# Kernel optimization log

Measured on AMD Instinct MI355X. Metric: run time of the kernel, lower is better.

Reference implementation:

```python
import jax, jax.numpy as jnp
import numpy as np

N = 50000       # total nodes
D = 20000       # disease nodes (first D rows)
M = 30000       # mirna nodes
E = 800000      # edges
DSIM = 512; MSIM = 512
HID = 128; OUT = 128; P = 3   # powers p = [0,1,2]
PAIRS = 100000


def _lin(k, o, i):
    s = 1.0 / np.sqrt(i)
    return jax.random.uniform(k, (o, i), jnp.float32, -s, s)


def setup_inputs() -> dict:
    key = jax.random.key(0)
    ks = jax.random.split(key, 24)
    inp = {}
    inp["d_sim"] = jax.random.normal(ks[0], (N, DSIM), jnp.float32)
    inp["m_sim"] = jax.random.normal(ks[1], (N, MSIM), jnp.float32)
    inp["edge_src"] = jax.random.randint(ks[2], (E,), 0, N, jnp.int32)
    inp["edge_dst"] = jax.random.randint(ks[3], (E,), 0, N, jnp.int32)
    inp["src"] = jax.random.randint(ks[4], (PAIRS,), 0, D, jnp.int32)
    inp["dst"] = D + jax.random.randint(ks[5], (PAIRS,), 0, M, jnp.int32)
    # input projections
    inp["d_fc_w"] = _lin(ks[6], HID, DSIM); inp["d_fc_b"] = jnp.zeros((HID,), jnp.float32)
    inp["m_fc_w"] = _lin(ks[7], HID, MSIM); inp["m_fc_b"] = jnp.zeros((HID,), jnp.float32)
    # MixHopConv per-power weights (no bias)
    inp["l0_w"] = jnp.stack([_lin(ks[8 + j], OUT, HID) for j in range(P)])         # [P, OUT, HID]
    inp["l1_w"] = jnp.stack([_lin(ks[11 + j], HID, OUT * P) for j in range(P)])    # [P, HID, OUT*P]
    inp["fc_w"] = _lin(ks[14], OUT, HID * P)
    inp["d_fc1_w"] = _lin(ks[15], OUT, OUT + DSIM); inp["d_fc1_b"] = jnp.zeros((OUT,), jnp.float32)
    inp["m_fc1_w"] = _lin(ks[16], OUT, OUT + MSIM); inp["m_fc1_b"] = jnp.zeros((OUT,), jnp.float32)
    # predictor MLP
    inp["p0_w"] = _lin(ks[17], OUT, 2 * OUT); inp["p0_b"] = jnp.zeros((OUT,), jnp.float32)
    inp["p1_w"] = _lin(ks[18], 1, OUT); inp["p1_b"] = jnp.zeros((1,), jnp.float32)
    return inp


def _mixhop(feats, Ws, edge_src, edge_dst, norm):
    """DGL MixHopConv with p=[0,1,2]: outputs [W_j (D^-1/2 A D^-1/2)^j X for j in p], concatenated."""
    outs = []
    for j in range(P):
        outs.append(feats @ Ws[j].T)
        if j < P - 1:  # propagate one more hop (last hop's propagation is unused)
            feats = feats * norm
            feats = jax.ops.segment_sum(feats[edge_src], edge_dst, num_segments=N)
            feats = feats * norm
    return jnp.concatenate(outs, axis=1)


def reference(d_sim, m_sim, edge_src, edge_dst, src, dst,
              d_fc_w, d_fc_b, m_fc_w, m_fc_b, l0_w, l1_w, fc_w,
              d_fc1_w, d_fc1_b, m_fc1_w, m_fc1_b, p0_w, p0_b, p1_w, p1_b):
    # symmetric normalization from in-degrees (clamped to >= 1)
    degs = jax.ops.segment_sum(jnp.ones((E,), jnp.float32), edge_dst, num_segments=N)
    norm = (jnp.maximum(degs, 1.0) ** -0.5)[:, None]  # [N, 1]
    # per-node-type input projection (dropout = identity in eval)
    z_d = d_sim[:D] @ d_fc_w.T + d_fc_b
    z_m = m_sim[D:] @ m_fc_w.T + m_fc_b
    feats = jnp.concatenate([z_d, z_m], axis=0)               # [N, HID]
    feats = _mixhop(feats, l0_w, edge_src, edge_dst, norm)    # [N, OUT*P]
    feats = _mixhop(feats, l1_w, edge_src, edge_dst, norm)    # [N, HID*P]
    feats = feats @ fc_w.T                                    # [N, OUT]
    h_d = jax.nn.elu(jnp.concatenate([feats[:D], d_sim[:D]], axis=1) @ d_fc1_w.T + d_fc1_b)
    h_m = jax.nn.elu(jnp.concatenate([feats[D:], m_sim[D:]], axis=1) @ m_fc1_w.T + m_fc1_b)
    h = jnp.concatenate([h_d, h_m], axis=0)                   # [N, OUT]
    hc = jnp.concatenate([h[src], h[dst]], axis=1)            # [PAIRS, 2*OUT]
    score = jax.nn.sigmoid(jax.nn.relu(hc @ p0_w.T + p0_b) @ p1_w.T + p1_b)
    return score
```

## Files before the change

kernel.cpp:

```cpp
#include <hip/hip_runtime.h>
#include <cstddef>
#include <cstdint>

#define N_NODES 50000
#define D_NODES 20000
#define M_NODES 30000
#define E_EDGES 800000
#define PAIRS_N 100000

typedef unsigned short u16;
typedef unsigned int u32;
typedef short bf16x8 __attribute__((ext_vector_type(8)));
typedef float f32x4 __attribute__((ext_vector_type(4)));

__device__ __forceinline__ float bf2f(u16 u) {
  u32 v = ((u32)u) << 16;
  return __builtin_bit_cast(float, v);
}
__device__ __forceinline__ u16 f2bf(float f) {
  u32 u = __builtin_bit_cast(u32, f);
  u32 r = (u + 0x7fffu + ((u >> 16) & 1u)) >> 16;
  return (u16)r;
}
__device__ __forceinline__ u32 pk2(float x, float y) {
  return (u32)f2bf(x) | ((u32)f2bf(y) << 16);
}

__global__ void wconv_kernel(const float* s0, const float* s1, const float* s2,
                             const float* s3, const float* s4,
                             u16* d0, u16* d1, u16* d2, u16* d3, u16* d4) {
  int i = blockIdx.x * 256 + threadIdx.x;
  const float* s; u16* d; int l;
  if      (i < 16384) { s = s0; d = d0; l = i; }
  else if (i < 32768) { s = s1; d = d1; l = i - 16384; }
  else if (i < 53248) { s = s2; d = d2; l = i - 32768; }
  else if (i < 73728) { s = s3; d = d3; l = i - 53248; }
  else if (i < 81920) { s = s4; d = d4; l = i - 73728; }
  else return;
  float4 v = *(const float4*)(s + (size_t)l * 4);
  ushort4 o;
  o.x = f2bf(v.x); o.y = f2bf(v.y); o.z = f2bf(v.z); o.w = f2bf(v.w);
  *(ushort4*)(d + (size_t)l * 4) = o;
}

__global__ void wcomb1_kernel(const float* __restrict__ l1w, const float* __restrict__ l0w,
                              float* __restrict__ Tmp) {
  int pj = blockIdx.x;
  int p = pj / 3, j = pj % 3;
  int o = blockIdx.y;
  int i = threadIdx.x;
  const float* wp = l1w + (size_t)p * 49152 + (size_t)o * 384 + 128 * j;
  const float* wj = l0w + (size_t)j * 16384 + i;
  float acc = 0.f;
#pragma unroll 4
  for (int t = 0; t < 128; ++t) acc += wp[t] * wj[(size_t)t * 128];
  Tmp[(size_t)pj * 16384 + (size_t)o * 128 + i] = acc;
}
__global__ void wcomb2_kernel(const float* __restrict__ fcw, const float* __restrict__ Tmp,
                              u16* __restrict__ G) {
  int k = blockIdx.x;
  int of = blockIdx.y;
  int i = threadIdx.x;
  float acc = 0.f;
  int plo = (k > 2) ? (k - 2) : 0;
  int phi = (k < 2) ? k : 2;
  for (int p = plo; p <= phi; ++p) {
    int j = k - p;
    const float* fp = fcw + (size_t)of * 384 + 128 * p;
    const float* tp = Tmp + (size_t)(p * 3 + j) * 16384 + i;
#pragma unroll 4
    for (int t = 0; t < 128; ++t) acc += fp[t] * tp[(size_t)t * 128];
  }
  G[(size_t)of * 640 + 128 * k + i] = f2bf(acc);
}

__global__ void deg_count_kernel(const int* __restrict__ dst, int* __restrict__ degs, int e) {
  int i = blockIdx.x * 256 + threadIdx.x;
  if (i < e) atomicAdd(&degs[dst[i]], 1);
}
__global__ void norm_reduce_kernel(const int* __restrict__ degs, float* __restrict__ norm,
                                   int n, int* __restrict__ bsums) {
  __shared__ int s[256];
  int t = threadIdx.x;
  int i = blockIdx.x * 256 + t;
  int d = (i < n) ? degs[i] : 0;
  if (i < n) norm[i] = rsqrtf(fmaxf((float)d, 1.0f));
  s[t] = d;
  __syncthreads();
  for (int st = 128; st > 0; st >>= 1) {
    if (t < st) s[t] += s[t + st];
    __syncthreads();
  }
  if (t == 0) bsums[blockIdx.x] = s[0];
}
__global__ void scan_small_kernel(int* b, int nb) {
  __shared__ int s[256];
  int t = threadIdx.x;
  int orig = (t < nb) ? b[t] : 0;
  s[t] = orig;
  __syncthreads();
  for (int st = 1; st < 256; st <<= 1) {
    int v = (t >= st) ? s[t - st] : 0;
    __syncthreads();
    s[t] += v;
    __syncthreads();
  }
  if (t < nb) b[t] = s[t] - orig;
}
__global__ void scan_final_kernel(const int* __restrict__ degs, const int* __restrict__ boff,
                                  int* __restrict__ out, int* __restrict__ cursor,
                                  int n, int total) {
  __shared__ int s[256];
  int t = threadIdx.x;
  int i = blockIdx.x * 256 + t;
  int orig = (i < n) ? degs[i] : 0;
  s[t] = orig;
  __syncthreads();
  for (int st = 1; st < 256; st <<= 1) {
    int v = (t >= st) ? s[t - st] : 0;
    __syncthreads();
    s[t] += v;
    __syncthreads();
  }
  if (i < n) {
    int v = boff[blockIdx.x] + s[t] - orig;
    out[i] = v;
    cursor[i] = v;
  }
  if (i == 0) out[n] = total;
}
__global__ void fill_csr_kernel(const int* __restrict__ esrc, const int* __restrict__ edst,
                                int* __restrict__ cursor, int* __restrict__ csr_src, int e) {
  int i = blockIdx.x * 256 + threadIdx.x;
  if (i < e) {
    int p = atomicAdd(&cursor[edst[i]], 1);
    csr_src[p] = esrc[i];
  }
}

__global__ void prop_kernel(const u16* __restrict__ in,
                            u16* __restrict__ outu, int ldu, int cOff,
                            u16* __restrict__ outs,
                            const int* __restrict__ off, const int* __restrict__ srcs,
                            const float* __restrict__ norm, int nnodes) {
  const int node = blockIdx.x * 4 + (threadIdx.x >> 6);
  if (node >= nnodes) return;
  const int lane = threadIdx.x & 63;
  const int e0 = off[node], e1 = off[node + 1];
  float a0 = 0.f, a1 = 0.f;
  const u16* basec = in + (lane << 1);
  for (int base = e0; base < e1; base += 64) {
    int nE = e1 - base; if (nE > 64) nE = 64;
    int myE = srcs[base + ((lane < nE) ? lane : (nE - 1))];
    int i = 0;
    for (; i + 8 <= nE; i += 8) {
      int s0 = __builtin_amdgcn_readlane(myE, i + 0);
      int s1 = __builtin_amdgcn_readlane(myE, i + 1);
      int s2 = __builtin_amdgcn_readlane(myE, i + 2);
      int s3 = __builtin_amdgcn_readlane(myE, i + 3);
      int s4 = __builtin_amdgcn_readlane(myE, i + 4);
      int s5 = __builtin_amdgcn_readlane(myE, i + 5);
      int s6 = __builtin_amdgcn_readlane(myE, i + 6);
      int s7 = __builtin_amdgcn_readlane(myE, i + 7);
      u32 v0 = *(const u32*)(basec + ((size_t)s0 << 7));
      u32 v1 = *(const u32*)(basec + ((size_t)s1 << 7));
      u32 v2 = *(const u32*)(basec + ((size_t)s2 << 7));
      u32 v3 = *(const u32*)(basec + ((size_t)s3 << 7));
      u32 v4 = *(const u32*)(basec + ((size_t)s4 << 7));
      u32 v5 = *(const u32*)(basec + ((size_t)s5 << 7));
      u32 v6 = *(const u32*)(basec + ((size_t)s6 << 7));
      u32 v7 = *(const u32*)(basec + ((size_t)s7 << 7));
      a0 += bf2f((u16)v0); a1 += bf2f((u16)(v0 >> 16));
      a0 += bf2f((u16)v1); a1 += bf2f((u16)(v1 >> 16));
      a0 += bf2f((u16)v2); a1 += bf2f((u16)(v2 >> 16));
      a0 += bf2f((u16)v3); a1 += bf2f((u16)(v3 >> 16));
      a0 += bf2f((u16)v4); a1 += bf2f((u16)(v4 >> 16));
      a0 += bf2f((u16)v5); a1 += bf2f((u16)(v5 >> 16));
      a0 += bf2f((u16)v6); a1 += bf2f((u16)(v6 >> 16));
      a0 += bf2f((u16)v7); a1 += bf2f((u16)(v7 >> 16));
    }
    for (; i < nE; ++i) {
      int s = __builtin_amdgcn_readlane(myE, i);
      u32 v = *(const u32*)(basec + ((size_t)s << 7));
      a0 += bf2f((u16)v); a1 += bf2f((u16)(v >> 16));
    }
  }
  float nd = norm[node];
  *(u32*)(outu + (size_t)node * ldu + cOff + (lane << 1)) = pk2(a0 * nd, a1 * nd);
  if (outs) {
    float nd2 = nd * nd;
    *(u32*)(outs + ((size_t)node << 7) + (lane << 1)) = pk2(a0 * nd2, a1 * nd2);
  }
}

__global__ __launch_bounds__(256) void mfma_gemm_kernel(
    const void* __restrict__ A1a, const void* __restrict__ A1b, int lda1, int K1, int a1f32,
    const void* __restrict__ A2a, const void* __restrict__ A2b, int lda2, int K2, int a2f32,
    const int* __restrict__ gsrc, const int* __restrict__ gdst,
    const u16* __restrict__ Wa, const u16* __restrict__ Wb,
    const float* __restrict__ biasa, const float* __restrict__ biasb,
    int splitB, int rowD, int boundA, int nrows,
    u16* __restrict__ Cu, int ldcu, int colOff,
    u16* __restrict__ Cs, const float* __restrict__ normp,
    const float* __restrict__ p1w, const float* __restrict__ p1b, float* __restrict__ outf,
    int act) {
  __shared__ u32 As[32 * 32];
  __shared__ u32 Ws[128 * 32];
  const int tid = threadIdx.x;
  const bool segb = (int)blockIdx.x >= splitB;
  const int brow = segb ? rowD + ((int)blockIdx.x - splitB) * 32 : (int)blockIdx.x * 32;
  const int bound = segb ? nrows : boundA;
  const void* A1 = segb ? A1b : A1a;
  const void* A2 = segb ? A2b : A2a;
  const u16* W = segb ? Wb : Wa;
  const float* bias = segb ? biasb : biasa;
  const int K = K1 + K2;
  const int lane = tid & 63;
  const int wv = tid >> 6;
  const int fr = lane & 15;
  const int fg = lane >> 4;

  f32x4 acc[2][2];
#pragma unroll
  for (int m = 0; m < 2; ++m)
#pragma unroll
    for (int n = 0; n < 2; ++n) acc[m][n] = (f32x4){0.f, 0.f, 0.f, 0.f};

  const int sr = tid >> 3, sk = tid & 7;
  const int swc = tid >> 1, sh = tid & 1;
  const int prow = (brow + sr < bound) ? (brow + sr) : (bound - 1);

  for (int kc = 0; kc < K; kc += 64) {
    uint4 qa;
    {
      bool seg1 = kc < K1;
      int kk = (seg1 ? kc : kc - K1) + sk * 8;
      const void* Av = seg1 ? A1 : A2;
      int ld = seg1 ? lda1 : lda2;
      int isf = seg1 ? a1f32 : a2f32;
      int row = gsrc ? (seg1 ? gsrc[prow] : gdst[prow]) : prow;
      if (isf) {
        const float* p = (const float*)Av + (size_t)row * ld + kk;
        float4 f0 = ((const float4*)p)[0];
        float4 f1 = ((const float4*)p)[1];
        qa = make_uint4(pk2(f0.x, f0.y), pk2(f0.z, f0.w), pk2(f1.x, f1.y), pk2(f1.z, f1.w));
      } else {
        qa = *(const uint4*)((const u16*)Av + (size_t)row * ld + kk);
      }
    }
    const u16* wp = W + (size_t)swc * K + kc + sh * 32;
    uint4 qw0 = *(const uint4*)(wp);
    uint4 qw1 = *(const uint4*)(wp + 8);
    uint4 qw2 = *(const uint4*)(wp + 16);
    uint4 qw3 = *(const uint4*)(wp + 24);

    __syncthreads();
    *(uint4*)&As[sr * 32 + (sk ^ (sr & 7)) * 4] = qa;
    *(uint4*)&Ws[swc * 32 + ((sh * 4 + 0) ^ (swc & 7)) * 4] = qw0;
    *(uint4*)&Ws[swc * 32 + ((sh * 4 + 1) ^ (swc & 7)) * 4] = qw1;
    *(uint4*)&Ws[swc * 32 + ((sh * 4 + 2) ^ (swc & 7)) * 4] = qw2;
    *(uint4*)&Ws[swc * 32 + ((sh * 4 + 3) ^ (swc & 7)) * 4] = qw3;
    __syncthreads();

#pragma unroll
    for (int kk2 = 0; kk2 < 2; ++kk2) {
      int gix = kk2 * 4 + fg;
      int r0 = fr, r1 = 16 + fr;
      bf16x8 aF0 = *(const bf16x8*)&As[r0 * 32 + (gix ^ (r0 & 7)) * 4];
      bf16x8 aF1 = *(const bf16x8*)&As[r1 * 32 + (gix ^ (r1 & 7)) * 4];
#pragma unroll
      for (int n = 0; n < 2; ++n) {
        int cr = wv * 32 + n * 16 + fr;
        bf16x8 bF = *(const bf16x8*)&Ws[cr * 32 + (gix ^ (cr & 7)) * 4];
        acc[0][n] = __builtin_amdgcn_mfma_f32_16x16x32_bf16(aF0, bF, acc[0][n], 0, 0, 0);
        acc[1][n] = __builtin_amdgcn_mfma_f32_16x16x32_bf16(aF1, bF, acc[1][n], 0, 0, 0);
      }
    }
  }

  if (act == 3) {
    float part[2][4];
#pragma unroll
    for (int m = 0; m < 2; ++m)
#pragma unroll
      for (int i = 0; i < 4; ++i) part[m][i] = 0.f;
#pragma unroll
    for (int n = 0; n < 2; ++n) {
      int ccol = wv * 32 + n * 16 + fr;
      float b = bias[ccol];
      float pw = p1w[ccol];
#pragma unroll
      for (int m = 0; m < 2; ++m)
#pragma unroll
        for (int i = 0; i < 4; ++i) {
          float v = acc[m][n][i] + b;
          v = fmaxf(v, 0.f);
          part[m][i] += v * pw;
        }
    }
#pragma unroll
    for (int mask = 1; mask <= 8; mask <<= 1)
#pragma unroll
      for (int m = 0; m < 2; ++m)
#pragma unroll
        for (int i = 0; i < 4; ++i) part[m][i] += __shfl_xor(part[m][i], mask);
    __syncthreads();
    float* sred = (float*)As;
    if (fr == 0) {
#pragma unroll
      for (int m = 0; m < 2; ++m)
#pragma unroll
        for (int i = 0; i < 4; ++i) sred[wv * 32 + m * 16 + fg * 4 + i] = part[m][i];
    }
    __syncthreads();
    if (tid < 32) {
      int row = brow + tid;
      if (row < bound) {
        float s = sred[tid] + sred[32 + tid] + sred[64 + tid] + sred[96 + tid] + p1b[0];
        outf[row] = 1.f / (1.f + expf(-s));
      }
    }
    return;
  }

#pragma unroll
  for (int m = 0; m < 2; ++m) {
#pragma unroll
    for (int n = 0; n < 2; ++n) {
      int ccol = wv * 32 + n * 16 + fr;
      float b = bias ? bias[ccol] : 0.f;
#pragma unroll
      for (int i = 0; i < 4; ++i) {
        int row = brow + m * 16 + fg * 4 + i;
        if (row < bound) {
          float v = acc[m][n][i] + b;
          if (act == 1) v = (v > 0.f) ? v : (expf(v) - 1.f);
          else if (act == 2) v = fmaxf(v, 0.f);
          Cu[(size_t)row * ldcu + colOff + ccol] = f2bf(v);
          if (Cs) Cs[((size_t)row << 7) + ccol] = f2bf(v * normp[row]);
        }
      }
    }
  }
}

extern "C" void kernel_launch(void* const* d_in, const int* in_sizes, int n_in,
                              void* d_out, int out_size, void* d_ws, size_t ws_size,
                              hipStream_t stream) {
  const float* d_sim   = (const float*)d_in[0];
  const float* m_sim   = (const float*)d_in[1];
  const int*   e_src   = (const int*)d_in[2];
  const int*   e_dst   = (const int*)d_in[3];
  const int*   p_src   = (const int*)d_in[4];
  const int*   p_dst   = (const int*)d_in[5];
  const float* d_fc_w  = (const float*)d_in[6];
  const float* d_fc_b  = (const float*)d_in[7];
  const float* m_fc_w  = (const float*)d_in[8];
  const float* m_fc_b  = (const float*)d_in[9];
  const float* l0_w    = (const float*)d_in[10];
  const float* l1_w    = (const float*)d_in[11];
  const float* fc_w    = (const float*)d_in[12];
  const float* d_fc1_w = (const float*)d_in[13];
  const float* d_fc1_b = (const float*)d_in[14];
  const float* m_fc1_w = (const float*)d_in[15];
  const float* m_fc1_b = (const float*)d_in[16];
  const float* p0_w    = (const float*)d_in[17];
  const float* p0_b    = (const float*)d_in[18];
  const float* p1_w    = (const float*)d_in[19];
  const float* p1_b    = (const float*)d_in[20];
  float* out = (float*)d_out;

  const int N = N_NODES, D = D_NODES, M = M_NODES, E = E_EDGES, NP = PAIRS_N;

  u16* ws16 = (u16*)d_ws;
  u16* HCAT = ws16;
  u16* HSa  = HCAT + (size_t)N * 640;
  u16* HSb  = HSa + (size_t)N * 128;
  u16* FE   = HSb + (size_t)N * 128;
  u16* HB   = FE  + (size_t)N * 128;
  u16* wb_dfc  = HB + (size_t)N * 128;
  u16* wb_mfc  = wb_dfc  + 65536;
  u16* wb_dfc1 = wb_mfc  + 65536;
  u16* wb_mfc1 = wb_dfc1 + 81920;
  u16* wb_p0   = wb_mfc1 + 81920;
  u16* wb_G    = wb_p0   + 32768;
  u16* wend    = wb_G    + 81920;
  size_t off16 = (size_t)(wend - ws16);
  off16 = (off16 + 1) & ~(size_t)1;
  float* Tmp   = (float*)(ws16 + off16);
  float* normp = Tmp + 9 * 16384;
  int* degs    = (int*)(normp + N);
  int* csr_off = degs + N;
  int* cursor  = csr_off + N + 1;
  int* csr_src = cursor + N;
  int* bsums   = csr_src + E;

  const int nb = (N + 255) / 256;
  const int eb = (E + 255) / 256;

  wconv_kernel<<<320, 256, 0, stream>>>(d_fc_w, m_fc_w, d_fc1_w, m_fc1_w, p0_w,
                                        wb_dfc, wb_mfc, wb_dfc1, wb_mfc1, wb_p0);
  wcomb1_kernel<<<dim3(9, 128), 128, 0, stream>>>(l1_w, l0_w, Tmp);
  wcomb2_kernel<<<dim3(5, 128), 128, 0, stream>>>(fc_w, Tmp, wb_G);

  hipMemsetAsync(degs, 0, (size_t)N * 4, stream);
  deg_count_kernel<<<eb, 256, 0, stream>>>(e_dst, degs, E);
  norm_reduce_kernel<<<nb, 256, 0, stream>>>(degs, normp, N, bsums);
  scan_small_kernel<<<1, 256, 0, stream>>>(bsums, nb);
  scan_final_kernel<<<nb, 256, 0, stream>>>(degs, bsums, csr_off, cursor, N, E);
  fill_csr_kernel<<<eb, 256, 0, stream>>>(e_src, e_dst, cursor, csr_src, E);

  const int GDseg = D / 32;
  const int GMseg = (M + 31) / 32;
  const int GSEG = GDseg + GMseg;
  const int GN = (N + 31) / 32;
  const int GP = (NP + 31) / 32;
  const int GPROP = (N + 3) / 4;

  mfma_gemm_kernel<<<GSEG, 256, 0, stream>>>(
      d_sim, m_sim, 512, 512, 1, nullptr, nullptr, 0, 0, 0, nullptr, nullptr,
      wb_dfc, wb_mfc, d_fc_b, m_fc_b, GDseg, D, D, N,
      HCAT, 640, 0, HSa, normp, nullptr, nullptr, nullptr, 0);

  prop_kernel<<<GPROP, 256, 0, stream>>>(HSa, HCAT, 640, 128, HSb, csr_off, csr_src, normp, N);
  prop_kernel<<<GPROP, 256, 0, stream>>>(HSb, HCAT, 640, 256, HSa, csr_off, csr_src, normp, N);
  prop_kernel<<<GPROP, 256, 0, stream>>>(HSa, HCAT, 640, 384, HSb, csr_off, csr_src, normp, N);
  prop_kernel<<<GPROP, 256, 0, stream>>>(HSb, HCAT, 640, 512, nullptr, csr_off, csr_src, normp, N);

  mfma_gemm_kernel<<<GN, 256, 0, stream>>>(
      HCAT, HCAT, 640, 640, 0, nullptr, nullptr, 0, 0, 0, nullptr, nullptr,
      wb_G, wb_G, nullptr, nullptr, GN, 0, N, N,
      FE, 128, 0, nullptr, normp, nullptr, nullptr, nullptr, 0);

  mfma_gemm_kernel<<<GSEG, 256, 0, stream>>>(
      FE, FE, 128, 128, 0, d_sim, m_sim, 512, 512, 1, nullptr, nullptr,
      wb_dfc1, wb_mfc1, d_fc1_b, m_fc1_b, GDseg, D, D, N,
      HB, 128, 0, nullptr, normp, nullptr, nullptr, nullptr, 1);

  mfma_gemm_kernel<<<GP, 256, 0, stream>>>(
      HB, HB, 128, 128, 0, HB, HB, 128, 128, 0, p_src, p_dst,
      wb_p0, wb_p0, p0_b, p0_b, GP, 0, NP, NP,
      nullptr, 128, 0, nullptr, normp, p1_w, p1_b, out, 3);

  (void)in_sizes; (void)n_in; (void)out_size; (void)ws_size;
}
```

Baseline: 379.1 us.

## Rewrite MFMA GEMM to load fragments directly from global, 64-row tiles

The GEMM kernel drops LDS staging and both per-K-step barriers; each wave now loads its A and B MFMA fragments straight from global memory and computes a 32x64 sub-tile, so a block covers 64 rows by 128 columns. Grid sizes are recomputed for 64-row blocks. The predictor reduction now combines only two column halves. The memset is replaced by a small zero kernel. This removes LDS traffic and sync stalls, but weights are no longer shared across waves through LDS, so global and L2 read traffic for W rises, and fragment loads are strided per lane.

```diff
diff --git a/kernel.cpp b/kernel.cpp
--- a/kernel.cpp
+++ b/kernel.cpp
@@ -24,6 +24,10 @@
 }
 __device__ __forceinline__ u32 pk2(float x, float y) {
   return (u32)f2bf(x) | ((u32)f2bf(y) << 16);
+}
+__device__ __forceinline__ bf16x8 pk8(float4 a, float4 b) {
+  uint4 q = make_uint4(pk2(a.x, a.y), pk2(a.z, a.w), pk2(b.x, b.y), pk2(b.z, b.w));
+  return __builtin_bit_cast(bf16x8, q);
 }
 
 __global__ void wconv_kernel(const float* s0, const float* s1, const float* s2,
@@ -74,6 +78,10 @@
   G[(size_t)of * 640 + 128 * k + i] = f2bf(acc);
 }
 
+__global__ void zero_int_kernel(int* p, int n) {
+  int i = blockIdx.x * 256 + threadIdx.x;
+  if (i < n) p[i] = 0;
+}
 __global__ void deg_count_kernel(const int* __restrict__ dst, int* __restrict__ degs, int e) {
   int i = blockIdx.x * 256 + threadIdx.x;
   if (i < e) atomicAdd(&degs[dst[i]], 1);
@@ -204,77 +212,77 @@
     u16* __restrict__ Cs, const float* __restrict__ normp,
     const float* __restrict__ p1w, const float* __restrict__ p1b, float* __restrict__ outf,
     int act) {
-  __shared__ u32 As[32 * 32];
-  __shared__ u32 Ws[128 * 32];
+  __shared__ float sred[2][64];
   const int tid = threadIdx.x;
+  const int w = tid >> 6, lane = tid & 63;
+  const int ch = w & 1, rg = w >> 1;
+  const int fr = lane & 15, fg = lane >> 4;
   const bool segb = (int)blockIdx.x >= splitB;
-  const int brow = segb ? rowD + ((int)blockIdx.x - splitB) * 32 : (int)blockIdx.x * 32;
+  const int brow = segb ? rowD + ((int)blockIdx.x - splitB) * 64 : (int)blockIdx.x * 64;
   const int bound = segb ? nrows : boundA;
   const void* A1 = segb ? A1b : A1a;
   const void* A2 = segb ? A2b : A2a;
   const u16* W = segb ? Wb : Wa;
   const float* bias = segb ? biasb : biasa;
   const int K = K1 + K2;
-  const int lane = tid & 63;
-  const int wv = tid >> 6;
-  const int fr = lane & 15;
-  const int fg = lane >> 4;
-
-  f32x4 acc[2][2];
+
+  int r0 = brow + rg * 32 + fr;
+  int r1 = r0 + 16;
+  int c0 = (r0 < bound) ? r0 : (bound - 1);
+  int c1 = (r1 < bound) ? r1 : (bound - 1);
+  int gA0, gA1, gB0, gB1;
+  if (gsrc) { gA0 = gsrc[c0]; gA1 = gsrc[c1]; gB0 = gdst[c0]; gB1 = gdst[c1]; }
+  else { gA0 = c0; gA1 = c1; gB0 = c0; gB1 = c1; }
+
+  const u16* wbase = W + (size_t)(ch * 64 + fr) * K + fg * 8;
+
+  f32x4 acc[2][4];
 #pragma unroll
   for (int m = 0; m < 2; ++m)
 #pragma unroll
-    for (int n = 0; n < 2; ++n) acc[m][n] = (f32x4){0.f, 0.f, 0.f, 0.f};
-
-  const int sr = tid >> 3, sk = tid & 7;
-  const int swc = tid >> 1, sh = tid & 1;
-  const int prow = (brow + sr < bound) ? (brow + sr) : (bound - 1);
+    for (int n = 0; n < 4; ++n) acc[m][n] = (f32x4){0.f, 0.f, 0.f, 0.f};
 
   for (int kc = 0; kc < K; kc += 64) {
-    uint4 qa;
-    {
-      bool seg1 = kc < K1;
-      int kk = (seg1 ? kc : kc - K1) + sk * 8;
-      const void* Av = seg1 ? A1 : A2;
-      int ld = seg1 ? lda1 : lda2;
-      int isf = seg1 ? a1f32 : a2f32;
-      int row = gsrc ? (seg1 ? gsrc[prow] : gdst[prow]) : prow;
-      if (isf) {
-        const float* p = (const float*)Av + (size_t)row * ld + kk;
-        float4 f0 = ((const float4*)p)[0];
-        float4 f1 = ((const float4*)p)[1];
-        qa = make_uint4(pk2(f0.x, f0.y), pk2(f0.z, f0.w), pk2(f1.x, f1.y), pk2(f1.z, f1.w));
-      } else {
-        qa = *(const uint4*)((const u16*)Av + (size_t)row * ld + kk);
-      }
-    }
-    const u16* wp = W + (size_t)swc * K + kc + sh * 32;
-    uint4 qw0 = *(const uint4*)(wp);
-    uint4 qw1 = *(const uint4*)(wp + 8);
-    uint4 qw2 = *(const uint4*)(wp + 16);
-    uint4 qw3 = *(const uint4*)(wp + 24);
-
-    __syncthreads();
-    *(uint4*)&As[sr * 32 + (sk ^ (sr & 7)) * 4] = qa;
-    *(uint4*)&Ws[swc * 32 + ((sh * 4 + 0) ^ (swc & 7)) * 4] = qw0;
-    *(uint4*)&Ws[swc * 32 + ((sh * 4 + 1) ^ (swc & 7)) * 4] = qw1;
-    *(uint4*)&Ws[swc * 32 + ((sh * 4 + 2) ^ (swc & 7)) * 4] = qw2;
-    *(uint4*)&Ws[swc * 32 + ((sh * 4 + 3) ^ (swc & 7)) * 4] = qw3;
-    __syncthreads();
-
-#pragma unroll
-    for (int kk2 = 0; kk2 < 2; ++kk2) {
-      int gix = kk2 * 4 + fg;
-      int r0 = fr, r1 = 16 + fr;
-      bf16x8 aF0 = *(const bf16x8*)&As[r0 * 32 + (gix ^ (r0 & 7)) * 4];
-      bf16x8 aF1 = *(const bf16x8*)&As[r1 * 32 + (gix ^ (r1 & 7)) * 4];
-#pragma unroll
-      for (int n = 0; n < 2; ++n) {
-        int cr = wv * 32 + n * 16 + fr;
-        bf16x8 bF = *(const bf16x8*)&Ws[cr * 32 + (gix ^ (cr & 7)) * 4];
-        acc[0][n] = __builtin_amdgcn_mfma_f32_16x16x32_bf16(aF0, bF, acc[0][n], 0, 0, 0);
-        acc[1][n] = __builtin_amdgcn_mfma_f32_16x16x32_bf16(aF1, bF, acc[1][n], 0, 0, 0);
-      }
+    const bool seg1 = kc < K1;
+    const int kk = (seg1 ? kc : kc - K1) + fg * 8;
+    const int ld = seg1 ? lda1 : lda2;
+    const int isf = seg1 ? a1f32 : a2f32;
+    const void* Av = seg1 ? A1 : A2;
+    const int ra = seg1 ? gA0 : gB0;
+    const int rb = seg1 ? gA1 : gB1;
+
+    bf16x8 aAh0, aAh1, aBh0, aBh1;
+    if (isf) {
+      const float* pa = (const float*)Av + (size_t)ra * ld + kk;
+      const float* pb = (const float*)Av + (size_t)rb * ld + kk;
+      float4 a00 = ((const float4*)pa)[0], a01 = ((const float4*)pa)[1];
+      float4 a10 = ((const float4*)(pa + 32))[0], a11 = ((const float4*)(pa + 32))[1];
+      float4 b00 = ((const float4*)pb)[0], b01 = ((const float4*)pb)[1];
+      float4 b10 = ((const float4*)(pb + 32))[0], b11 = ((const float4*)(pb + 32))[1];
+      aAh0 = pk8(a00, a01); aAh1 = pk8(a10, a11);
+      aBh0 = pk8(b00, b01); aBh1 = pk8(b10, b11);
+    } else {
+      const u16* pa = (const u16*)Av + (size_t)ra * ld + kk;
+      const u16* pb = (const u16*)Av + (size_t)rb * ld + kk;
+      aAh0 = *(const bf16x8*)pa; aAh1 = *(const bf16x8*)(pa + 32);
+      aBh0 = *(const bf16x8*)pb; aBh1 = *(const bf16x8*)(pb + 32);
+    }
+    bf16x8 bh0[4], bh1[4];
+#pragma unroll
+    for (int n = 0; n < 4; ++n) {
+      const u16* wp = wbase + (size_t)n * 16 * K + kc;
+      bh0[n] = *(const bf16x8*)wp;
+      bh1[n] = *(const bf16x8*)(wp + 32);
+    }
+#pragma unroll
+    for (int n = 0; n < 4; ++n) {
+      acc[0][n] = __builtin_amdgcn_mfma_f32_16x16x32_bf16(aAh0, bh0[n], acc[0][n], 0, 0, 0);
+      acc[1][n] = __builtin_amdgcn_mfma_f32_16x16x32_bf16(aBh0, bh0[n], acc[1][n], 0, 0, 0);
+    }
+#pragma unroll
+    for (int n = 0; n < 4; ++n) {
+      acc[0][n] = __builtin_amdgcn_mfma_f32_16x16x32_bf16(aAh1, bh1[n], acc[0][n], 0, 0, 0);
+      acc[1][n] = __builtin_amdgcn_mfma_f32_16x16x32_bf16(aBh1, bh1[n], acc[1][n], 0, 0, 0);
     }
   }
 
@@ -285,16 +293,15 @@
 #pragma unroll
       for (int i = 0; i < 4; ++i) part[m][i] = 0.f;
 #pragma unroll
-    for (int n = 0; n < 2; ++n) {
-      int ccol = wv * 32 + n * 16 + fr;
+    for (int n = 0; n < 4; ++n) {
+      int ccol = ch * 64 + n * 16 + fr;
       float b = bias[ccol];
       float pw = p1w[ccol];
 #pragma unroll
       for (int m = 0; m < 2; ++m)
 #pragma unroll
         for (int i = 0; i < 4; ++i) {
-          float v = acc[m][n][i] + b;
-          v = fmaxf(v, 0.f);
+          float v = fmaxf(acc[m][n][i] + b, 0.f);
           part[m][i] += v * pw;
         }
     }
@@ -304,19 +311,17 @@
       for (int m = 0; m < 2; ++m)
 #pragma unroll
         for (int i = 0; i < 4; ++i) part[m][i] += __shfl_xor(part[m][i], mask);
-    __syncthreads();
-    float* sred = (float*)As;
     if (fr == 0) {
 #pragma unroll
       for (int m = 0; m < 2; ++m)
 #pragma unroll
-        for (int i = 0; i < 4; ++i) sred[wv * 32 + m * 16 + fg * 4 + i] = part[m][i];
-    }
-    __syncthreads();
-    if (tid < 32) {
+        for (int i = 0; i < 4; ++i) sred[ch][rg * 32 + m * 16 + fg * 4 + i] = part[m][i];
+    }
+    __syncthreads();
+    if (tid < 64) {
       int row = brow + tid;
       if (row < bound) {
-        float s = sred[tid] + sred[32 + tid] + sred[64 + tid] + sred[96 + tid] + p1b[0];
+        float s = sred[0][tid] + sred[1][tid] + p1b[0];
         outf[row] = 1.f / (1.f + expf(-s));
       }
     }
@@ -326,16 +331,15 @@
 #pragma unroll
   for (int m = 0; m < 2; ++m) {
 #pragma unroll
-    for (int n = 0; n < 2; ++n) {
-      int ccol = wv * 32 + n * 16 + fr;
+    for (int n = 0; n < 4; ++n) {
+      int ccol = ch * 64 + n * 16 + fr;
       float b = bias ? bias[ccol] : 0.f;
 #pragma unroll
       for (int i = 0; i < 4; ++i) {
-        int row = brow + m * 16 + fg * 4 + i;
+        int row = brow + rg * 32 + m * 16 + fg * 4 + i;
         if (row < bound) {
           float v = acc[m][n][i] + b;
           if (act == 1) v = (v > 0.f) ? v : (expf(v) - 1.f);
-          else if (act == 2) v = fmaxf(v, 0.f);
           Cu[(size_t)row * ldcu + colOff + ccol] = f2bf(v);
           if (Cs) Cs[((size_t)row << 7) + ccol] = f2bf(v * normp[row]);
         }
@@ -403,18 +407,18 @@
   wcomb1_kernel<<<dim3(9, 128), 128, 0, stream>>>(l1_w, l0_w, Tmp);
   wcomb2_kernel<<<dim3(5, 128), 128, 0, stream>>>(fc_w, Tmp, wb_G);
 
-  hipMemsetAsync(degs, 0, (size_t)N * 4, stream);
+  zero_int_kernel<<<nb, 256, 0, stream>>>(degs, N);
   deg_count_kernel<<<eb, 256, 0, stream>>>(e_dst, degs, E);
   norm_reduce_kernel<<<nb, 256, 0, stream>>>(degs, normp, N, bsums);
   scan_small_kernel<<<1, 256, 0, stream>>>(bsums, nb);
   scan_final_kernel<<<nb, 256, 0, stream>>>(degs, bsums, csr_off, cursor, N, E);
   fill_csr_kernel<<<eb, 256, 0, stream>>>(e_src, e_dst, cursor, csr_src, E);
 
-  const int GDseg = D / 32;
-  const int GMseg = (M + 31) / 32;
+  const int GDseg = (D + 63) / 64;
+  const int GMseg = (M + 63) / 64;
   const int GSEG = GDseg + GMseg;
-  const int GN = (N + 31) / 32;
-  const int GP = (NP + 31) / 32;
+  const int GN = (N + 63) / 64;
+  const int GP = (NP + 63) / 64;
   const int GPROP = (N + 3) / 4;
 
   mfma_gemm_kernel<<<GSEG, 256, 0, stream>>>(
```

Result: slower. 522.6 us (+37.8%).
